# Kernel optimization log

Measured on AMD Instinct MI355X. Metric: run time of the kernel, lower is better.

## Reference

```python
import jax, jax.numpy as jnp
import numpy as np

B, P, H, NO, NA = 8, 16, 32, 32, 8
D, L, NH, F = 768, 12, 12, 3072
DH = D // NH
N = P + H * (NO + NA)  # 1296
NEG = -1e9


def _rule_mask():
    # group ids: 0=task(prefix), 1=obs, 2=action; prefix timestep = -1
    g = np.concatenate([np.zeros(P, np.int32),
                        np.tile(np.concatenate([np.full(NO, 1, np.int32), np.full(NA, 2, np.int32)]), H)])
    t = np.concatenate([np.full(P, -1, np.int32), np.repeat(np.arange(H, dtype=np.int32), NO + NA)])
    ti, tj = t[:, None], t[None, :]
    # attention_rules: everyone attends ALL to task; obs/action attend CAUSAL to obs;
    # action attends CAUSAL to action; task attends ALL to task; all else NEVER.
    rules = {(0, 0): 'all', (1, 0): 'all', (2, 0): 'all',
             (1, 1): 'causal', (2, 1): 'causal', (2, 2): 'causal'}
    m = np.zeros((N, N), bool)
    for (gi, gj), r in rules.items():
        sel = (g[:, None] == gi) & (g[None, :] == gj)
        cond = np.ones((N, N), bool) if r == 'all' else (tj <= ti)
        m |= sel & cond
    return m

RULE_MASK = jnp.asarray(_rule_mask())
SCALE = np.float32(1.0 / np.sqrt(DH))


def _ln(x, s, b):
    mu = x.mean(-1, keepdims=True)
    var = ((x - mu) ** 2).mean(-1, keepdims=True)
    return (x - mu) * jax.lax.rsqrt(var + 1e-6) * s + b


def _forward(prefix_tokens, obs_tokens, act_tokens, ln1_s, ln1_b, ln2_s, ln2_b,
             wq, wk, wv, wo, bq, bk, bv, bo, w1, b1, w2, b2, lnf_s, lnf_b,
             prefix_mask, obs_mask, act_mask):
    # assemble_input_tokens: concat timestep groups on token dim, fold horizon, prepend prefix
    ts = jnp.concatenate([obs_tokens, act_tokens], axis=2).reshape(B, H * (NO + NA), D)
    x = jnp.concatenate([prefix_tokens, ts], axis=1)  # (B, N, D)
    pad = jnp.concatenate(
        [prefix_mask, jnp.concatenate([obs_mask, act_mask], axis=2).reshape(B, -1)], axis=1)
    mask = RULE_MASK[None, None] & pad[:, None, None, :]  # (B,1,N,N), broadcast over heads
    for i in range(L):
        h = _ln(x, ln1_s[i], ln1_b[i])
        q = (h @ wq[i] + bq[i]).reshape(B, N, NH, DH)
        k = (h @ wk[i] + bk[i]).reshape(B, N, NH, DH)
        v = (h @ wv[i] + bv[i]).reshape(B, N, NH, DH)
        s = jnp.einsum('bqhd,bkhd->bhqk', q, k) * SCALE
        a = jax.nn.softmax(jnp.where(mask, s, NEG), axis=-1)
        o = jnp.einsum('bhqk,bkhd->bqhd', a, v).reshape(B, N, D)
        x = x + o @ wo[i] + bo[i]
        h2 = _ln(x, ln2_s[i], ln2_b[i])
        x = x + jax.nn.gelu(h2 @ w1[i] + b1[i]) @ w2[i] + b2[i]
    return _ln(x, lnf_s, lnf_b)


def setup_inputs() -> dict:
    key = jax.random.key(0)
    ks = jax.random.split(key, 9)
    sc = 0.02
    return dict(
        prefix_tokens=jax.random.normal(ks[0], (B, P, D), jnp.float32),
        obs_tokens=jax.random.normal(ks[1], (B, H, NO, D), jnp.float32),
        act_tokens=jax.random.normal(ks[2], (B, H, NA, D), jnp.float32),
        ln1_s=jnp.ones((L, D), jnp.float32), ln1_b=jnp.zeros((L, D), jnp.float32),
        ln2_s=jnp.ones((L, D), jnp.float32), ln2_b=jnp.zeros((L, D), jnp.float32),
        wq=jax.random.normal(ks[3], (L, D, D), jnp.float32) * sc,
        wk=jax.random.normal(ks[4], (L, D, D), jnp.float32) * sc,
        wv=jax.random.normal(ks[5], (L, D, D), jnp.float32) * sc,
        wo=jax.random.normal(ks[6], (L, D, D), jnp.float32) * sc,
        bq=jnp.zeros((L, D), jnp.float32), bk=jnp.zeros((L, D), jnp.float32),
        bv=jnp.zeros((L, D), jnp.float32), bo=jnp.zeros((L, D), jnp.float32),
        w1=jax.random.normal(ks[7], (L, D, F), jnp.float32) * sc,
        b1=jnp.zeros((L, F), jnp.float32),
        w2=jax.random.normal(ks[8], (L, F, D), jnp.float32) * sc,
        b2=jnp.zeros((L, D), jnp.float32),
        lnf_s=jnp.ones((D,), jnp.float32), lnf_b=jnp.zeros((D,), jnp.float32),
        prefix_mask=jnp.ones((B, P), bool),
        obs_mask=jnp.ones((B, H, NO), bool),
        act_mask=jnp.ones((B, H, NA), bool),
    )


def reference(prefix_tokens, obs_tokens, act_tokens, ln1_s, ln1_b, ln2_s, ln2_b,
              wq, wk, wv, wo, bq, bk, bv, bo, w1, b1, w2, b2, lnf_s, lnf_b,
              prefix_mask, obs_mask, act_mask):
    return _forward(prefix_tokens, obs_tokens, act_tokens, ln1_s, ln1_b, ln2_s, ln2_b,
                    wq, wk, wv, wo, bq, bk, bv, bo, w1, b1, w2, b2, lnf_s, lnf_b,
                    prefix_mask, obs_mask, act_mask)
```

## Files before the change

kernel.cpp:

```cpp
#include <hip/hip_runtime.h>

typedef unsigned short u16;
typedef __attribute__((ext_vector_type(8))) __bf16 bf16x8;
typedef __attribute__((ext_vector_type(4))) float floatx4;

#define NTOK 1296
#define BN_TOT 10368
#define DMODEL 768
#define DFF 3072
#define NHEAD 12
#define DHEAD 64
#define NLAYER 12
#define NQT 21
#define SCALE_QK 0.125f

__device__ __forceinline__ u16 f2bf(float f) {
    unsigned u = __builtin_bit_cast(unsigned, f);
    unsigned r = (u + 0x7FFFu + ((u >> 16) & 1u)) >> 16;
    return (u16)r;
}

__device__ __forceinline__ unsigned cvt_pk_bf16(float lo, float hi) {
    unsigned r;
    asm("v_cvt_pk_bf16_f32 %0, %1, %2" : "=v"(r) : "v"(lo), "v"(hi));
    return r;
}

__device__ __forceinline__ float gelu_f(float x) {
    float u = 0.7978845608028654f * (x + 0.044715f * x * x * x);
    float t = 1.f - 2.f / (__expf(2.f * u) + 1.f);
    return 0.5f * x * (1.f + t);
}

__global__ void assemble_x(const float* __restrict__ prefix,
                           const float* __restrict__ obs,
                           const float* __restrict__ act,
                           float* __restrict__ X) {
    int idx = blockIdx.x * 256 + threadIdx.x;
    if (idx >= BN_TOT * DMODEL) return;
    int d = idx % DMODEL;
    int n = (idx / DMODEL) % NTOK;
    int b = idx / (DMODEL * NTOK);
    float v;
    if (n < 16) {
        v = prefix[((size_t)b * 16 + n) * DMODEL + d];
    } else {
        int q = n - 16;
        int m = q / 40, r = q % 40;
        if (r < 32) v = obs[(((size_t)b * 32 + m) * 32 + r) * DMODEL + d];
        else        v = act[(((size_t)b * 32 + m) * 8 + (r - 32)) * DMODEL + d];
    }
    X[idx] = v;
}

__global__ void build_pad(const int* __restrict__ pm,
                          const int* __restrict__ om,
                          const int* __restrict__ am,
                          unsigned char* __restrict__ pad) {
    int idx = blockIdx.x * 256 + threadIdx.x;
    if (idx >= BN_TOT) return;
    int n = idx % NTOK, b = idx / NTOK;
    int v;
    if (n < 16) v = pm[b * 16 + n];
    else {
        int q = n - 16;
        int m = q / 40, r = q % 40;
        v = (r < 32) ? om[(b * 32 + m) * 32 + r] : am[(b * 32 + m) * 8 + (r - 32)];
    }
    pad[idx] = (v != 0) ? 1 : 0;
}

__global__ void build_biascat(const float* __restrict__ bq,
                              const float* __restrict__ bk,
                              const float* __restrict__ bv,
                              float* __restrict__ bc) {
    int idx = blockIdx.x * 256 + threadIdx.x;
    if (idx >= NLAYER * 2304) return;
    int l = idx / 2304, c = idx % 2304;
    int which = c / 768, cc = c % 768;
    const float* src = (which == 0) ? bq : (which == 1) ? bk : bv;
    bc[idx] = src[l * 768 + cc];
}

__global__ void transpose_cvt(const float* __restrict__ src, u16* __restrict__ dst,
                              int K, int Nc, long layerStride) {
    src += (size_t)blockIdx.z * K * Nc;
    dst += (size_t)blockIdx.z * layerStride;
    __shared__ float tile[32][33];
    int n0 = blockIdx.x * 32, k0 = blockIdx.y * 32;
    int tx = threadIdx.x, ty = threadIdx.y;
#pragma unroll
    for (int i = 0; i < 4; ++i)
        tile[ty + i * 8][tx] = src[(size_t)(k0 + ty + i * 8) * Nc + n0 + tx];
    __syncthreads();
#pragma unroll
    for (int i = 0; i < 4; ++i) {
        int n = n0 + ty + i * 8;
        dst[(size_t)n * K + k0 + tx] = f2bf(tile[tx][ty + i * 8]);
    }
}

__global__ __launch_bounds__(256) void ln_kernel(const float* __restrict__ x,
                                                 const float* __restrict__ s,
                                                 const float* __restrict__ bb,
                                                 u16* __restrict__ obf,
                                                 float* __restrict__ of32) {
    int row = blockIdx.x * 4 + (threadIdx.x >> 6);
    int lane = threadIdx.x & 63;
    const float4* xv = (const float4*)(x + (size_t)row * DMODEL);
    float4 v[3];
    v[0] = xv[lane]; v[1] = xv[lane + 64]; v[2] = xv[lane + 128];
    float sum = 0.f, sq = 0.f;
#pragma unroll
    for (int i = 0; i < 3; ++i) {
        sum += v[i].x + v[i].y + v[i].z + v[i].w;
        sq  += v[i].x * v[i].x + v[i].y * v[i].y + v[i].z * v[i].z + v[i].w * v[i].w;
    }
#pragma unroll
    for (int d = 32; d > 0; d >>= 1) {
        sum += __shfl_xor(sum, d);
        sq  += __shfl_xor(sq, d);
    }
    float mu = sum * (1.f / DMODEL);
    float var = sq * (1.f / DMODEL) - mu * mu;
    float rstd = rsqrtf(var + 1e-6f);
    const float4* sv = (const float4*)s;
    const float4* bv = (const float4*)bb;
#pragma unroll
    for (int i = 0; i < 3; ++i) {
        float4 sc = sv[lane + i * 64], bc = bv[lane + i * 64];
        float y0 = (v[i].x - mu) * rstd * sc.x + bc.x;
        float y1 = (v[i].y - mu) * rstd * sc.y + bc.y;
        float y2 = (v[i].z - mu) * rstd * sc.z + bc.z;
        float y3 = (v[i].w - mu) * rstd * sc.w + bc.w;
        size_t base = (size_t)row * DMODEL + i * 256 + lane * 4;
        if (obf) {
            uint2 pk;
            pk.x = (unsigned)f2bf(y0) | ((unsigned)f2bf(y1) << 16);
            pk.y = (unsigned)f2bf(y2) | ((unsigned)f2bf(y3) << 16);
            *(uint2*)&obf[base] = pk;
        } else {
            float4 o = {y0, y1, y2, y3};
            *(float4*)&of32[base] = o;
        }
    }
}

template <int EPI>
__global__ __launch_bounds__(256) void gemm_k(const u16* __restrict__ A,
                                              const u16* __restrict__ Bt,
                                              const float* __restrict__ bias,
                                              const float* __restrict__ resid,
                                              void* __restrict__ outp,
                                              int M, int Nc, int K) {
    __shared__ __attribute__((aligned(16))) u16 As[4096];
    __shared__ __attribute__((aligned(16))) u16 Bs[4096];
    int tid = threadIdx.x;
    int bc = blockIdx.x, br = blockIdx.y;
    int lane = tid & 63, w = tid >> 6;
    int wr = (w >> 1) * 64, wc = (w & 1) * 64;
    int lr = lane & 15, C = lane >> 4;
    floatx4 acc[4][4] = {};

    int r0 = tid >> 2;
    int cph = tid & 3;
    const u16* Abase = A + (size_t)(br * 128) * K;
    const u16* Bbase = Bt + (size_t)(bc * 128) * K;

    for (int k0 = 0; k0 < K; k0 += 32) {
        __syncthreads();
#pragma unroll
        for (int i = 0; i < 2; ++i) {
            int r = i * 64 + r0;
            int cl = cph ^ ((r >> 1) & 3);
            const u16* ga = Abase + (size_t)r * K + k0 + cl * 8;
            const u16* gb = Bbase + (size_t)r * K + k0 + cl * 8;
            __builtin_amdgcn_global_load_lds(
                (const __attribute__((address_space(1))) void*)ga,
                (__attribute__((address_space(3))) void*)&As[(i * 256 + w * 64) * 8], 16, 0, 0);
            __builtin_amdgcn_global_load_lds(
                (const __attribute__((address_space(1))) void*)gb,
                (__attribute__((address_space(3))) void*)&Bs[(i * 256 + w * 64) * 8], 16, 0, 0);
        }
        __syncthreads();
        bf16x8 af[4], bf[4];
#pragma unroll
        for (int i = 0; i < 4; ++i) {
            int R = wr + i * 16 + lr;
            af[i] = *(const bf16x8*)&As[(R * 4 + (C ^ ((R >> 1) & 3))) * 8];
        }
#pragma unroll
        for (int i = 0; i < 4; ++i) {
            int R = wc + i * 16 + lr;
            bf[i] = *(const bf16x8*)&Bs[(R * 4 + (C ^ ((R >> 1) & 3))) * 8];
        }
#pragma unroll
        for (int i = 0; i < 4; ++i)
#pragma unroll
            for (int j = 0; j < 4; ++j)
                acc[i][j] = __builtin_amdgcn_mfma_f32_16x16x32_bf16(af[i], bf[j], acc[i][j], 0, 0, 0);
    }

    int gr0 = br * 128 + wr, gc0 = bc * 128 + wc;
#pragma unroll
    for (int i = 0; i < 4; ++i) {
#pragma unroll
        for (int j = 0; j < 4; ++j) {
#pragma unroll
            for (int r = 0; r < 4; ++r) {
                int grow = gr0 + i * 16 + (lane >> 4) * 4 + r;
                int gcol = gc0 + j * 16 + lr;
                float v = acc[i][j][r] + bias[gcol];
                if constexpr (EPI == 2) {
                    ((u16*)outp)[(size_t)grow * Nc + gcol] = f2bf(gelu_f(v));
                } else if constexpr (EPI == 3) {
                    size_t idx = (size_t)grow * Nc + gcol;
                    ((float*)outp)[idx] = resid[idx] + v;
                } else {
                    int b = grow / NTOK, n = grow % NTOK;
                    int which = gcol / 768;
                    int c = gcol - which * 768;
                    int nh = c >> 6, dh = c & 63;
                    u16* base = (u16*)outp + (size_t)which * ((size_t)BN_TOT * DMODEL);
                    if (which < 2)
                        base[(((size_t)b * NHEAD + nh) * NTOK + n) * DHEAD + dh] = f2bf(v);
                    else
                        base[(((size_t)b * NHEAD + nh) * DHEAD + dh) * NTOK + n] = f2bf(v);
                }
            }
        }
    }
}

__global__ __launch_bounds__(256) void attn_k(const u16* __restrict__ Q,
                                              const u16* __restrict__ Kb,
                                              const u16* __restrict__ Vt,
                                              const unsigned char* __restrict__ pad,
                                              u16* __restrict__ O) {
    __shared__ __attribute__((aligned(16))) u16 plds[4][16 * 64];
    int wgid = blockIdx.x;
    int xcd = wgid & 7, slot = wgid >> 3;
    int qt = NQT - 1 - (slot % NQT);
    int g = (slot / NQT) * 8 + xcd;
    int b = g / NHEAD, h = g % NHEAD;

    int tid = threadIdx.x, lane = tid & 63, w = tid >> 6;
    int rg = lane >> 4, lc = lane & 15;
    int q0 = qt * 64 + w * 16;
    size_t bh = (size_t)(b * NHEAD + h);

    int lastrow = min(qt * 64 + 63, NTOK - 1);
    int jend = (lastrow < 16) ? 16 : 16 + 40 * ((lastrow - 16) / 40 + 1);
    jend = min(jend, NTOK);
    int njt = (jend + 63) >> 6;

    int q = q0 + lc;
    bool qok = q < NTOK;
    int tmax_obs = -1, tmax_act = -1;
    if (qok && q >= 16) {
        int qi = q - 16;
        int ti = qi / 40;
        bool gact = (qi % 40) >= 32;
        tmax_obs = ti;
        tmax_act = gact ? ti : -1;
    }

    const u16* qb = Q + (bh * NTOK + min(q, NTOK - 1)) * DHEAD;
    bf16x8 qf0, qf1;
    {
        bf16x8 t0 = *(const bf16x8*)(qb + rg * 8);
        bf16x8 t1 = *(const bf16x8*)(qb + 32 + rg * 8);
#pragma unroll
        for (int i = 0; i < 8; ++i) {
            qf0[i] = (__bf16)((float)t0[i] * SCALE_QK);
            qf1[i] = (__bf16)((float)t1[i] * SCALE_QK);
        }
    }

    floatx4 oacc[4] = {};
    float mi = -3.0e38f, li = 0.f;
    const unsigned char* padb = pad + (size_t)b * NTOK;

    for (int jt = 0; jt < njt; ++jt) {
        int j0 = jt * 64;
        floatx4 s[4];
#pragma unroll
        for (int ct = 0; ct < 4; ++ct) {
            int keyc = min(j0 + ct * 16 + lc, NTOK - 1);
            const u16* kb = Kb + (bh * NTOK + keyc) * DHEAD;
            bf16x8 kf0 = *(const bf16x8*)(kb + rg * 8);
            bf16x8 kf1 = *(const bf16x8*)(kb + 32 + rg * 8);
            floatx4 sa = {};
            sa = __builtin_amdgcn_mfma_f32_16x16x32_bf16(kf0, qf0, sa, 0, 0, 0);
            sa = __builtin_amdgcn_mfma_f32_16x16x32_bf16(kf1, qf1, sa, 0, 0, 0);
            s[ct] = sa;
        }
#pragma unroll
        for (int ct = 0; ct < 4; ++ct) {
            int kb0 = j0 + ct * 16 + rg * 4;
            unsigned pw = (kb0 < NTOK) ? *(const unsigned*)(padb + kb0) : 0u;
            bool jpre = kb0 < 16;
            int tj0 = 0, rem0 = 0;
            if (!jpre) { int qj = kb0 - 16; tj0 = qj / 40; rem0 = qj - 40 * tj0; }
#pragma unroll
            for (int r = 0; r < 4; ++r) {
                int key = kb0 + r;
                bool colok = qok && (key < jend) && (((pw >> (8 * r)) & 0xFFu) != 0);
                bool ok;
                if (jpre) ok = colok;
                else {
                    int rem = rem0 + r;
                    int tj = tj0 + (rem >= 40 ? 1 : 0);
                    int remr = rem >= 40 ? rem - 40 : rem;
                    int tm = (remr >= 32) ? tmax_act : tmax_obs;
                    ok = colok && (tj <= tm);
                }
                s[ct][r] = ok ? s[ct][r] : -1.0e9f;
            }
        }
        float mt = fmaxf(fmaxf(fmaxf(s[0][0], s[0][1]), fmaxf(s[0][2], s[0][3])),
                         fmaxf(fmaxf(s[1][0], s[1][1]), fmaxf(s[1][2], s[1][3])));
        float mt2 = fmaxf(fmaxf(fmaxf(s[2][0], s[2][1]), fmaxf(s[2][2], s[2][3])),
                          fmaxf(fmaxf(s[3][0], s[3][1]), fmaxf(s[3][2], s[3][3])));
        mt = fmaxf(mt, mt2);
        mt = fmaxf(mt, __shfl_xor(mt, 16));
        mt = fmaxf(mt, __shfl_xor(mt, 32));
        float mnew = fmaxf(mi, mt);
        float alpha = __expf(mi - mnew);
        float rs = 0.f;
#pragma unroll
        for (int ct = 0; ct < 4; ++ct)
#pragma unroll
            for (int r = 0; r < 4; ++r) {
                float p = __expf(s[ct][r] - mnew);
                s[ct][r] = p;
                rs += p;
            }
        rs += __shfl_xor(rs, 16);
        rs += __shfl_xor(rs, 32);
        li = li * alpha + rs;
        mi = mnew;
#pragma unroll
        for (int ct = 0; ct < 4; ++ct)
#pragma unroll
            for (int r = 0; r < 4; ++r) oacc[ct][r] *= alpha;
#pragma unroll
        for (int ct = 0; ct < 4; ++ct) {
            uint2 pk;
            pk.x = cvt_pk_bf16(s[ct][0], s[ct][1]);
            pk.y = cvt_pk_bf16(s[ct][2], s[ct][3]);
            int chunk = 2 * ct + (rg >> 1);
            int idx = lc * 64 + ((chunk ^ (lc & 7)) << 3) + ((rg & 1) << 2);
            *(uint2*)&plds[w][idx] = pk;
        }
#pragma unroll
        for (int kh = 0; kh < 2; ++kh) {
            bf16x8 pf = *(const bf16x8*)&plds[w][lc * 64 + (((4 * kh + rg) ^ (lc & 7)) << 3)];
#pragma unroll
            for (int ct = 0; ct < 4; ++ct) {
                const u16* vb = Vt + (bh * DHEAD + ct * 16 + lc) * NTOK + j0 + kh * 32;
                bf16x8 vf = *(const bf16x8*)(vb + rg * 8);
                oacc[ct] = __builtin_amdgcn_mfma_f32_16x16x32_bf16(vf, pf, oacc[ct], 0, 0, 0);
            }
        }
    }
    if (q < NTOK) {
        float inv = 1.f / li;
#pragma unroll
        for (int ct = 0; ct < 4; ++ct) {
            uint2 pk;
            pk.x = cvt_pk_bf16(oacc[ct][0] * inv, oacc[ct][1] * inv);
            pk.y = cvt_pk_bf16(oacc[ct][2] * inv, oacc[ct][3] * inv);
            *(uint2*)&O[((size_t)b * NTOK + q) * DMODEL + h * DHEAD + ct * 16 + rg * 4] = pk;
        }
    }
}

extern "C" void kernel_launch(void* const* d_in, const int* in_sizes, int n_in,
                              void* d_out, int out_size, void* d_ws, size_t ws_size,
                              hipStream_t stream) {
    const float* prefix = (const float*)d_in[0];
    const float* obs    = (const float*)d_in[1];
    const float* act    = (const float*)d_in[2];
    const float* ln1_s  = (const float*)d_in[3];
    const float* ln1_b  = (const float*)d_in[4];
    const float* ln2_s  = (const float*)d_in[5];
    const float* ln2_b  = (const float*)d_in[6];
    const float* wq = (const float*)d_in[7];
    const float* wk = (const float*)d_in[8];
    const float* wv = (const float*)d_in[9];
    const float* wo = (const float*)d_in[10];
    const float* bq = (const float*)d_in[11];
    const float* bk = (const float*)d_in[12];
    const float* bv = (const float*)d_in[13];
    const float* bo = (const float*)d_in[14];
    const float* w1 = (const float*)d_in[15];
    const float* b1 = (const float*)d_in[16];
    const float* w2 = (const float*)d_in[17];
    const float* b2 = (const float*)d_in[18];
    const float* lnf_s = (const float*)d_in[19];
    const float* lnf_b = (const float*)d_in[20];
    const int* pm = (const int*)d_in[21];
    const int* om = (const int*)d_in[22];
    const int* am = (const int*)d_in[23];
    float* out = (float*)d_out;

    char* ws = (char*)d_ws;
    size_t off = 0;
    auto carve = [&](size_t bytes) -> char* {
        char* p = ws + off;
        off += (bytes + 255) & ~(size_t)255;
        return p;
    };
    float* X   = (float*)carve((size_t)BN_TOT * DMODEL * 4);
    u16*   Hb  = (u16*)carve((size_t)BN_TOT * DMODEL * 2);
    u16*   QKV = (u16*)carve((size_t)3 * BN_TOT * DMODEL * 2);
    u16*   Qb  = QKV;
    u16*   Kbf = QKV + (size_t)BN_TOT * DMODEL;
    u16*   Vt  = QKV + (size_t)2 * BN_TOT * DMODEL;
    u16*   Ob  = (u16*)carve((size_t)BN_TOT * DMODEL * 2);
    u16*   MID = (u16*)carve((size_t)BN_TOT * DFF * 2);
    unsigned char* PAD = (unsigned char*)carve(BN_TOT);
    float* BIASC = (float*)carve((size_t)NLAYER * 2304 * 4);
    u16*   WT  = (u16*)carve((size_t)NLAYER * 7077888 * 2);
    if (off > ws_size) return;

    const long LSTR = 7077888;
    const long OWQ = 0, OWO = 1769472, OW1 = 2359296, OW2 = 4718592;
    const long OWK = 589824, OWV = 1179648;

    dim3 blk(256);
    assemble_x<<<(BN_TOT * DMODEL + 255) / 256, blk, 0, stream>>>(prefix, obs, act, X);
    build_pad<<<(BN_TOT + 255) / 256, blk, 0, stream>>>(pm, om, am, PAD);
    build_biascat<<<(NLAYER * 2304 + 255) / 256, blk, 0, stream>>>(bq, bk, bv, BIASC);

    dim3 tb(32, 8);
    transpose_cvt<<<dim3(DMODEL / 32, DMODEL / 32, NLAYER), tb, 0, stream>>>(wq, WT + OWQ, DMODEL, DMODEL, LSTR);
    transpose_cvt<<<dim3(DMODEL / 32, DMODEL / 32, NLAYER), tb, 0, stream>>>(wk, WT + OWK, DMODEL, DMODEL, LSTR);
    transpose_cvt<<<dim3(DMODEL / 32, DMODEL / 32, NLAYER), tb, 0, stream>>>(wv, WT + OWV, DMODEL, DMODEL, LSTR);
    transpose_cvt<<<dim3(DMODEL / 32, DMODEL / 32, NLAYER), tb, 0, stream>>>(wo, WT + OWO, DMODEL, DMODEL, LSTR);
    transpose_cvt<<<dim3(DFF / 32, DMODEL / 32, NLAYER), tb, 0, stream>>>(w1, WT + OW1, DMODEL, DFF, LSTR);
    transpose_cvt<<<dim3(DMODEL / 32, DFF / 32, NLAYER), tb, 0, stream>>>(w2, WT + OW2, DFF, DMODEL, LSTR);

    dim3 g6(DMODEL / 128, BN_TOT / 128);
    dim3 gqkv(2304 / 128, BN_TOT / 128);
    dim3 g24(DFF / 128, BN_TOT / 128);
    dim3 ga(NQT * NHEAD * 8);
    dim3 gln(BN_TOT / 4);

    for (int l = 0; l < NLAYER; ++l) {
        const u16* WTl = WT + (size_t)l * LSTR;
        ln_kernel<<<gln, blk, 0, stream>>>(X, ln1_s + l * DMODEL, ln1_b + l * DMODEL, Hb, nullptr);
        gemm_k<4><<<gqkv, blk, 0, stream>>>(Hb, WTl + OWQ, BIASC + l * 2304, nullptr, Qb, BN_TOT, 2304, DMODEL);
        attn_k<<<ga, blk, 0, stream>>>(Qb, Kbf, Vt, PAD, Ob);
        gemm_k<3><<<g6, blk, 0, stream>>>(Ob, WTl + OWO, bo + l * DMODEL, X, X, BN_TOT, DMODEL, DMODEL);
        ln_kernel<<<gln, blk, 0, stream>>>(X, ln2_s + l * DMODEL, ln2_b + l * DMODEL, Hb, nullptr);
        gemm_k<2><<<g24, blk, 0, stream>>>(Hb, WTl + OW1, b1 + l * DFF, nullptr, MID, BN_TOT, DFF, DMODEL);
        gemm_k<3><<<g6, blk, 0, stream>>>(MID, WTl + OW2, b2 + l * DMODEL, X, X, BN_TOT, DMODEL, DFF);
    }
    ln_kernel<<<gln, blk, 0, stream>>>(X, lnf_s, lnf_b, nullptr, out);
}
```

Measured before the change: 6.313 ms.

## Double-buffer K/V tiles in LDS via async global-to-LDS loads in attention

The attention kernel now stages each 64-key K tile and V^T tile into swizzled, double-buffered shared memory with global_load_lds. The next tile is prefetched while the current one is computed. Previously each of the four waves loaded the same K/V fragments straight from global memory, so this removes that redundant traffic and hides load latency. It also raises wave priority around the MFMA blocks, and it adds a block-wide barrier per tile plus extra LDS use that may reduce occupancy.

```diff
diff --git a/kernel.cpp b/kernel.cpp
--- a/kernel.cpp
+++ b/kernel.cpp
@@ -237,7 +237,10 @@
                                               const u16* __restrict__ Vt,
                                               const unsigned char* __restrict__ pad,
                                               u16* __restrict__ O) {
+    __shared__ __attribute__((aligned(16))) u16 Ks[2][64 * 64];
+    __shared__ __attribute__((aligned(16))) u16 Vs[2][64 * 64];
     __shared__ __attribute__((aligned(16))) u16 plds[4][16 * 64];
+
     int wgid = blockIdx.x;
     int xcd = wgid & 7, slot = wgid >> 3;
     int qt = NQT - 1 - (slot % NQT);
@@ -277,24 +280,48 @@
         }
     }
 
+    auto stage = [&](int buf, int jt) {
+#pragma unroll
+        for (int i = 0; i < 2; ++i) {
+            int r = i * 32 + (tid >> 3);
+            int cl = (tid & 7) ^ (r & 7);
+            const u16* gk = Kb + (bh * NTOK + min(jt * 64 + r, NTOK - 1)) * DHEAD + cl * 8;
+            const u16* gv = Vt + (bh * DHEAD + r) * NTOK + jt * 64 + cl * 8;
+            __builtin_amdgcn_global_load_lds(
+                (const __attribute__((address_space(1))) void*)gk,
+                (__attribute__((address_space(3))) void*)&Ks[buf][(i * 256 + w * 64) * 8], 16, 0, 0);
+            __builtin_amdgcn_global_load_lds(
+                (const __attribute__((address_space(1))) void*)gv,
+                (__attribute__((address_space(3))) void*)&Vs[buf][(i * 256 + w * 64) * 8], 16, 0, 0);
+        }
+    };
+
     floatx4 oacc[4] = {};
     float mi = -3.0e38f, li = 0.f;
     const unsigned char* padb = pad + (size_t)b * NTOK;
 
+    stage(0, 0);
+    __syncthreads();
+    int cur = 0;
+
     for (int jt = 0; jt < njt; ++jt) {
         int j0 = jt * 64;
+        if (jt + 1 < njt) stage(cur ^ 1, jt + 1);
+
         floatx4 s[4];
+        __builtin_amdgcn_s_setprio(1);
 #pragma unroll
         for (int ct = 0; ct < 4; ++ct) {
-            int keyc = min(j0 + ct * 16 + lc, NTOK - 1);
-            const u16* kb = Kb + (bh * NTOK + keyc) * DHEAD;
-            bf16x8 kf0 = *(const bf16x8*)(kb + rg * 8);
-            bf16x8 kf1 = *(const bf16x8*)(kb + 32 + rg * 8);
+            int kk = ct * 16 + lc;
+            bf16x8 kf0 = *(const bf16x8*)&Ks[cur][kk * 64 + ((rg ^ (lc & 7)) << 3)];
+            bf16x8 kf1 = *(const bf16x8*)&Ks[cur][kk * 64 + (((4 + rg) ^ (lc & 7)) << 3)];
             floatx4 sa = {};
             sa = __builtin_amdgcn_mfma_f32_16x16x32_bf16(kf0, qf0, sa, 0, 0, 0);
             sa = __builtin_amdgcn_mfma_f32_16x16x32_bf16(kf1, qf1, sa, 0, 0, 0);
             s[ct] = sa;
         }
+        __builtin_amdgcn_s_setprio(0);
+
 #pragma unroll
         for (int ct = 0; ct < 4; ++ct) {
             int kb0 = j0 + ct * 16 + rg * 4;
@@ -344,6 +371,7 @@
         for (int ct = 0; ct < 4; ++ct)
 #pragma unroll
             for (int r = 0; r < 4; ++r) oacc[ct][r] *= alpha;
+
 #pragma unroll
         for (int ct = 0; ct < 4; ++ct) {
             uint2 pk;
@@ -353,17 +381,23 @@
             int idx = lc * 64 + ((chunk ^ (lc & 7)) << 3) + ((rg & 1) << 2);
             *(uint2*)&plds[w][idx] = pk;
         }
+        __builtin_amdgcn_s_setprio(1);
 #pragma unroll
         for (int kh = 0; kh < 2; ++kh) {
             bf16x8 pf = *(const bf16x8*)&plds[w][lc * 64 + (((4 * kh + rg) ^ (lc & 7)) << 3)];
 #pragma unroll
             for (int ct = 0; ct < 4; ++ct) {
-                const u16* vb = Vt + (bh * DHEAD + ct * 16 + lc) * NTOK + j0 + kh * 32;
-                bf16x8 vf = *(const bf16x8*)(vb + rg * 8);
+                int dd = ct * 16 + lc;
+                bf16x8 vf = *(const bf16x8*)&Vs[cur][dd * 64 + (((kh * 4 + rg) ^ (lc & 7)) << 3)];
                 oacc[ct] = __builtin_amdgcn_mfma_f32_16x16x32_bf16(vf, pf, oacc[ct], 0, 0, 0);
             }
         }
-    }
+        __builtin_amdgcn_s_setprio(0);
+
+        __syncthreads();
+        cur ^= 1;
+    }
+
     if (q < NTOK) {
         float inv = 1.f / li;
 #pragma unroll
```

New measurement: 5.353 ms. 1.18x faster.
